# Kernel tuning notes

Measured on AMD Instinct MI355X. Metric: run time of the kernel, lower is better.

The kernel has to match this reference:

```python
import jax, jax.numpy as jnp
import numpy as np

V, NEIGH, C, N, H = 20000, 12, 16, 8, 4


def _circulant_basis(n):
    eye = jnp.eye(n, dtype=jnp.float32)
    return jnp.stack([jnp.roll(eye, b, axis=1) for b in range(n)])  # [n, n, n]


def setup_inputs() -> dict:
    key = jax.random.key(0)
    ks = jax.random.split(key, 12)
    x = jax.random.normal(ks[0], (V, C, N), dtype=jnp.float32)
    neighbors = jax.random.randint(ks[1], (V, NEIGH), 0, V)
    mask = jax.random.bernoulli(ks[2], 0.8, (V, NEIGH))
    pt = jax.random.normal(ks[3], (V, NEIGH, N, N), dtype=jnp.float32)
    rel_pos_u = jax.random.normal(ks[4], (V, NEIGH, 2), dtype=jnp.float32) * 0.1
    reg_basis = _circulant_basis(N)                                   # [N, N, N]
    value_basis1 = jax.random.normal(ks[5], (N, 2, N, N), dtype=jnp.float32)
    value_basis2 = jax.random.normal(ks[6], (N, 3, N, N), dtype=jnp.float32)
    s = 1.0 / np.sqrt(C * N)
    query_coeffs = jax.random.normal(ks[7], (H, C, N), dtype=jnp.float32) * s
    key_coeffs = jax.random.normal(ks[8], (H, C, N), dtype=jnp.float32) * s
    value0_params = jax.random.normal(ks[9], (H, C, N), dtype=jnp.float32) * s
    value1_params = jax.random.normal(ks[10], (H, C, N), dtype=jnp.float32) * s
    value2_params = jax.random.normal(ks[11], (H, C, N), dtype=jnp.float32) * s
    wm_weights = jax.random.normal(jax.random.fold_in(key, 99), (C, H * C, N), dtype=jnp.float32) * np.sqrt(2.0 / (H * C * N))
    return {"x": x, "neighbors": neighbors, "mask": mask,
            "parallel_transport_matrices": pt, "rel_pos_u": rel_pos_u,
            "reg_basis": reg_basis, "value_basis1": value_basis1,
            "value_basis2": value_basis2, "query_coeffs": query_coeffs,
            "key_coeffs": key_coeffs, "value0_params": value0_params,
            "value1_params": value1_params, "value2_params": value2_params,
            "wm_weights": wm_weights}


def reference(x, neighbors, mask, parallel_transport_matrices, rel_pos_u,
              reg_basis, value_basis1, value_basis2, query_coeffs, key_coeffs,
              value0_params, value1_params, value2_params, wm_weights):
    Nv, Cc, Nn = x.shape
    Hh = query_coeffs.shape[0]
    m = mask.astype(x.dtype)                                   # [v, n]
    x_neigh = x[neighbors] * m[:, :, None, None]               # [v, n, c, N]
    f = jnp.einsum('vnij,vncj->vnci', parallel_transport_matrices, x_neigh)
    # attention scores
    WQ = jnp.einsum('hcb,bij->hcij', query_coeffs, reg_basis)
    Q = jnp.einsum('hcij,vcj->vhi', WQ, x)                     # [v, h, N]
    WK = jnp.einsum('hcb,bij->hcij', key_coeffs, reg_basis)
    K = jnp.einsum('hcij,vncj->vnhi', WK, f)                   # [v, n, h, N]
    score = jax.nn.relu(Q[:, None] + K).mean(-1)               # [v, n, h]
    score = jnp.where(mask[:, :, None], score, 0.0)
    den = score.sum(axis=1)                                    # [v, h]
    dead = den < 1e-6
    n_valid = jnp.clip(m.sum(axis=1, keepdims=True), 1.0)      # [v, 1]
    uniform = m[:, :, None] / n_valid[:, :, None]              # [v, n, 1]
    attn = jnp.where(dead[:, None, :], uniform,
                     score / jnp.clip(den, 1e-6)[:, None, :])  # [v, n, h]
    # Taylor-basis values
    u0, u1 = rel_pos_u[..., 0], rel_pos_u[..., 1]
    u_quad = jnp.stack([u0 * u0, 2.0 * u0 * u1, u1 * u1], axis=-1)  # [v, n, 3]
    W0 = jnp.einsum('hcb,bij->hcij', value0_params, reg_basis)
    values = jnp.einsum('hcij,vncj->vnhci', W0, f)
    W1 = jnp.einsum('hcb,boij->hcoij', value1_params, value_basis1)
    values = values + jnp.einsum('hcoij,vncj,vno->vnhci', W1, f, rel_pos_u)
    W2 = jnp.einsum('hcb,boij->hcoij', value2_params, value_basis2)
    values = values + jnp.einsum('hcoij,vncj,vno->vnhci', W2, f, u_quad)
    head = jnp.einsum('vnh,vnhci->vhci', attn, values)         # [v, h, c, N]
    head = head.reshape(Nv, Hh * Cc, Nn)
    WM = jnp.einsum('ocb,bij->ocij', wm_weights, reg_basis)
    return jnp.einsum('ocij,vcj->voi', WM, head)               # [v, c, N]
```

## Files before the change

### kernel.cpp

```cpp
#include <hip/hip_runtime.h>

#define NV  20000
#define NNB 12
#define NC  16
#define NH  4
#define VC  4
#define GRID (NV/VC)

#define OFF_X    0
#define OFF_PT   528
#define OFF_HEAD 528
#define OFF_F    3792
#define OFF_QC   10128
#define OFF_KC   10656
#define OFF_Q    11184
#define OFF_SC   11312
#define OFF_DEN  11504
#define OFF_NV   11520
#define OFF_AT   11524
#define OFF_SCAL 11716
#define OFF_NB   12100
#define OFF_M    12148
#define SMEM_FL  12196

#define LD8(dst, off) { const float4 _a = *(const float4*)&smem[(off)]; \
                        const float4 _b = *(const float4*)&smem[(off)+4]; \
                        dst[0]=_a.x; dst[1]=_a.y; dst[2]=_a.z; dst[3]=_a.w; \
                        dst[4]=_b.x; dst[5]=_b.y; dst[6]=_b.z; dst[7]=_b.w; }
#define ST8(off, src) { *(float4*)&smem[(off)]   = make_float4(src[0],src[1],src[2],src[3]); \
                        *(float4*)&smem[(off)+4] = make_float4(src[4],src[5],src[6],src[7]); }

__global__ __launch_bounds__(256) void kdetect(const unsigned char* __restrict__ m,
                                               int* __restrict__ flag)
{
    __shared__ int s_nz;
    if (threadIdx.x == 0) s_nz = 0;
    __syncthreads();
    int nz = 0;
    for (int k = blockIdx.x * 256 + threadIdx.x; k < NV * NNB; k += gridDim.x * 256) {
        if ((k & 3) != 0 && m[k] != 0) nz = 1;
    }
    if (nz) atomicOr(&s_nz, 1);
    __syncthreads();
    if (threadIdx.x == 0 && s_nz) atomicOr(flag, 1);
}

__global__ __launch_bounds__(256) void ksetup(
    const float* __restrict__ v0p, const float* __restrict__ v1p,
    const float* __restrict__ v2p, const float* __restrict__ vb1,
    const float* __restrict__ vb2, float* __restrict__ A4)
{
    int idx = blockIdx.x * 256 + threadIdx.x;
    if (idx >= 24576) return;
    int j = idx & 7;
    int t = idx >> 3;
    int hc = t & 63; t >>= 6;
    int i = t & 7;
    int p = t >> 3;
    int h = hc >> 4, c = hc & 15;
    float s = 0.f;
    if (p == 0) {
        s = v0p[h*128 + c*8 + ((j - i + 8) & 7)];
    } else if (p <= 2) {
        int o = p - 1;
        #pragma unroll
        for (int b = 0; b < 8; ++b)
            s += v1p[h*128 + c*8 + b] * vb1[((b*2 + o)*8 + i)*8 + j];
    } else {
        int o = p - 3;
        #pragma unroll
        for (int b = 0; b < 8; ++b)
            s += v2p[h*128 + c*8 + b] * vb2[((b*3 + o)*8 + i)*8 + j];
    }
    A4[idx] = s;
}

__global__ __launch_bounds__(256) void kmain(
    const float* __restrict__ x, const int* __restrict__ nbr,
    const unsigned char* __restrict__ mskb, const float* __restrict__ pt,
    const float* __restrict__ rel, const float* __restrict__ qc,
    const float* __restrict__ kc, const float* __restrict__ A4,
    const float* __restrict__ wm, const int* __restrict__ flagp,
    float* __restrict__ out)
{
    const int tid = threadIdx.x;
    const int vbase = blockIdx.x * VC;
    const int bytemode = flagp[0];
    const int* mski = (const int*)mskb;

    __shared__ __align__(16) float smem[SMEM_FL];

    for (int k = tid; k < VC*128; k += 256)
        smem[OFF_X + (k>>7)*132 + (k&127)] = x[(vbase + (k>>7))*128 + (k&127)];
    for (int k = tid; k < VC*NNB*64; k += 256)
        smem[OFF_PT + (k>>6)*68 + (k&63)] = pt[vbase*(NNB*64) + k];
    for (int k = tid; k < 512; k += 256) {
        smem[OFF_QC + (k>>7)*132 + (k&127)] = qc[k];
        smem[OFF_KC + (k>>7)*132 + (k&127)] = kc[k];
    }
    if (tid < VC*NNB) {
        int gi = vbase*NNB + tid;
        ((int*)smem)[OFF_NB + tid] = nbr[gi];
        int raw = bytemode ? (int)mskb[gi] : mski[gi];
        smem[OFF_M + tid] = raw ? 1.0f : 0.0f;
    }
    if (tid >= 64 && tid < 64 + VC*NNB) {
        int vn = tid - 64;
        float u0 = rel[(vbase*NNB + vn)*2 + 0];
        float u1 = rel[(vbase*NNB + vn)*2 + 1];
        smem[OFF_SCAL+vn*8+0] = 1.0f;
        smem[OFF_SCAL+vn*8+1] = u0;
        smem[OFF_SCAL+vn*8+2] = u1;
        smem[OFF_SCAL+vn*8+3] = u0*u0;
        smem[OFF_SCAL+vn*8+4] = 2.0f*u0*u1;
        smem[OFF_SCAL+vn*8+5] = u1*u1;
        smem[OFF_SCAL+vn*8+6] = 0.0f;
        smem[OFF_SCAL+vn*8+7] = 0.0f;
    }
    __syncthreads();

    if (tid < 192) {
        const int vn = tid >> 2, cq = tid & 3;
        const int nb = ((const int*)smem)[OFF_NB + vn];
        const float m = smem[OFF_M + vn];
        const float4* xg = (const float4*)(x + nb*128 + cq*32);
        float xnf[32];
        #pragma unroll
        for (int q = 0; q < 8; ++q) {
            float4 tv = xg[q];
            xnf[q*4+0]=tv.x; xnf[q*4+1]=tv.y; xnf[q*4+2]=tv.z; xnf[q*4+3]=tv.w;
        }
        float acc[4][8];
        #pragma unroll
        for (int c4 = 0; c4 < 4; ++c4)
            #pragma unroll
            for (int i = 0; i < 8; ++i) acc[c4][i] = 0.f;
        #pragma unroll
        for (int i = 0; i < 8; ++i) {
            float pj[8]; LD8(pj, OFF_PT + vn*68 + i*8);
            #pragma unroll
            for (int c4 = 0; c4 < 4; ++c4)
                #pragma unroll
                for (int j = 0; j < 8; ++j)
                    acc[c4][i] += pj[j] * xnf[c4*8 + j];
        }
        #pragma unroll
        for (int c4 = 0; c4 < 4; ++c4) {
            int c = cq*4 + c4;
            float w[8];
            #pragma unroll
            for (int i = 0; i < 8; ++i) w[i] = m * acc[c4][i];
            ST8(OFF_F + vn*132 + c*8, w);
        }
    }
    __syncthreads();

    float K8[8] = {0,0,0,0,0,0,0,0};
    if (tid < 128) {
        const int cs = tid & 7, vh = tid >> 3, v = vh >> 2, h = vh & 3;
        float Q8[8] = {0,0,0,0,0,0,0,0};
        #pragma unroll
        for (int t = 0; t < 2; ++t) {
            int c = cs*2 + t;
            float xv[8]; LD8(xv, OFF_X + v*132 + c*8);
            float qv[8]; LD8(qv, OFF_QC + h*132 + c*8);
            #pragma unroll
            for (int s = 0; s < 8; ++s)
                #pragma unroll
                for (int i = 0; i < 8; ++i)
                    Q8[i] += qv[s] * xv[(i+s)&7];
        }
        #pragma unroll
        for (int msk = 1; msk < 8; msk <<= 1)
            #pragma unroll
            for (int i = 0; i < 8; ++i) Q8[i] += __shfl_xor(Q8[i], msk, 64);
        if (cs == 0) { ST8(OFF_Q + vh*8, Q8); }
    }
    if (tid < 192) {
        const int vn = tid >> 2, h = tid & 3;
        #pragma unroll 2
        for (int c = 0; c < 16; ++c) {
            float kv[8]; LD8(kv, OFF_KC + h*132 + c*8);
            float fv[8]; LD8(fv, OFF_F + vn*132 + c*8);
            #pragma unroll
            for (int s = 0; s < 8; ++s)
                #pragma unroll
                for (int i = 0; i < 8; ++i)
                    K8[i] += kv[s] * fv[(i+s)&7];
        }
    }
    __syncthreads();

    if (tid < 192) {
        const int vn = tid >> 2, h = tid & 3, v = vn / 12;
        float q[8]; LD8(q, OFF_Q + (v*4+h)*8);
        float s = 0.f;
        #pragma unroll
        for (int i = 0; i < 8; ++i) s += fmaxf(0.f, q[i] + K8[i]);
        smem[OFF_SC + vn*4 + h] = 0.125f * s * smem[OFF_M + vn];
    }
    __syncthreads();

    if (tid < 16) {
        int v = tid >> 2, h = tid & 3;
        float d = 0.f;
        for (int n = 0; n < 12; ++n) d += smem[OFF_SC + (v*12+n)*4 + h];
        smem[OFF_DEN + tid] = d;
        if (h == 0) {
            float nv = 0.f;
            for (int n = 0; n < 12; ++n) nv += smem[OFF_M + v*12 + n];
            smem[OFF_NV + v] = fmaxf(nv, 1.0f);
        }
    }
    __syncthreads();
    if (tid < 192) {
        const int vn = tid >> 2, h = tid & 3, v = vn / 12;
        float den = smem[OFF_DEN + v*4 + h];
        float at = (den < 1e-6f) ? (smem[OFF_M + vn] / smem[OFF_NV + v])
                                 : (smem[OFF_SC + vn*4 + h] / fmaxf(den, 1e-6f));
        smem[OFF_AT + vn*4 + h] = at;
    }
    __syncthreads();

    const int v6 = tid >> 6, h6 = (tid >> 4) & 3, c6 = tid & 15, hc = tid & 63;
    float G[6][8];
    #pragma unroll
    for (int p = 0; p < 6; ++p)
        #pragma unroll
        for (int j = 0; j < 8; ++j) G[p][j] = 0.f;
    for (int n = 0; n < 12; ++n) {
        int vn = v6*12 + n;
        float at = smem[OFF_AT + vn*4 + h6];
        float sc[8]; LD8(sc, OFF_SCAL + vn*8);
        float fv[8]; LD8(fv, OFF_F + vn*132 + c6*8);
        #pragma unroll
        for (int p = 0; p < 6; ++p) {
            float w = at * sc[p];
            #pragma unroll
            for (int j = 0; j < 8; ++j) G[p][j] += w * fv[j];
        }
    }
    float hd[8] = {0,0,0,0,0,0,0,0};
    #pragma unroll
    for (int p = 0; p < 6; ++p) {
        #pragma unroll
        for (int i = 0; i < 8; ++i) {
            const float4 a0 = *(const float4*)&A4[(((p*8+i)*64 + hc)*8)];
            const float4 a1 = *(const float4*)&A4[(((p*8+i)*64 + hc)*8) + 4];
            hd[i] += a0.x*G[p][0] + a0.y*G[p][1] + a0.z*G[p][2] + a0.w*G[p][3]
                   + a1.x*G[p][4] + a1.y*G[p][5] + a1.z*G[p][6] + a1.w*G[p][7];
        }
    }
    ST8(OFF_HEAD + v6*520 + hc*8, hd);
    __syncthreads();

    {
        const int v = tid >> 6, o = (tid >> 2) & 15, cs = tid & 3;
        float acc[8] = {0,0,0,0,0,0,0,0};
        #pragma unroll 2
        for (int cc = 0; cc < 16; ++cc) {
            int cp = cc*4 + cs;
            float hh[8]; LD8(hh, OFF_HEAD + v*520 + cp*8);
            const float4 w0 = *(const float4*)&wm[(o*64 + cp)*8];
            const float4 w1 = *(const float4*)&wm[(o*64 + cp)*8 + 4];
            float wv[8] = {w0.x,w0.y,w0.z,w0.w,w1.x,w1.y,w1.z,w1.w};
            #pragma unroll
            for (int d = 0; d < 8; ++d)
                #pragma unroll
                for (int i = 0; i < 8; ++i)
                    acc[i] += wv[d] * hh[(i+d)&7];
        }
        #pragma unroll
        for (int msk = 1; msk < 4; msk <<= 1)
            #pragma unroll
            for (int i = 0; i < 8; ++i) acc[i] += __shfl_xor(acc[i], msk, 64);
        if (cs == 0) {
            float* op = out + (vbase + v)*128 + o*8;
            *(float4*)op       = make_float4(acc[0],acc[1],acc[2],acc[3]);
            *(float4*)(op + 4) = make_float4(acc[4],acc[5],acc[6],acc[7]);
        }
    }
}

extern "C" void kernel_launch(void* const* d_in, const int* in_sizes, int n_in,
                              void* d_out, int out_size, void* d_ws, size_t ws_size,
                              hipStream_t stream)
{
    const float* x   = (const float*)d_in[0];
    const int*   nbr = (const int*)d_in[1];
    const unsigned char* msk = (const unsigned char*)d_in[2];
    const float* pt  = (const float*)d_in[3];
    const float* rel = (const float*)d_in[4];
    const float* vb1 = (const float*)d_in[6];
    const float* vb2 = (const float*)d_in[7];
    const float* qc  = (const float*)d_in[8];
    const float* kc  = (const float*)d_in[9];
    const float* v0p = (const float*)d_in[10];
    const float* v1p = (const float*)d_in[11];
    const float* v2p = (const float*)d_in[12];
    const float* wm  = (const float*)d_in[13];

    int*   flag = (int*)d_ws;
    float* A4   = (float*)d_ws + 64;
    float* outp = (float*)d_out;

    hipMemsetAsync(d_ws, 0, 256, stream);
    hipLaunchKernelGGL(kdetect, dim3(64),   dim3(256), 0, stream, msk, flag);
    hipLaunchKernelGGL(ksetup,  dim3(96),   dim3(256), 0, stream, v0p, v1p, v2p, vb1, vb2, A4);
    hipLaunchKernelGGL(kmain,   dim3(GRID), dim3(256), 0, stream,
                       x, nbr, msk, pt, rel, qc, kc, A4, wm, flag, outp);
}
```

Measured before the change: 321.9 us.

## Shrink LDS footprint via buffer aliasing and merge prep kernels into one launch

Reorganizes the shared-memory layout so the parallel-transport staging area is reused for the query/key coefficients, Q and head buffers, and the attention weights overwrite the score buffer. x is now read directly from global memory instead of being staged, and the scalar basis array is compacted. Together these cut LDS per block so that four blocks can fit per CU, which launch_bounds(256,4) now requests. The mask-detect and basis-setup kernels are merged into one launch to save launch overhead. The cost is an extra barrier, a __syncthreads inside a branch that is only safe because the split falls on wave boundaries, and tighter register limits.

```diff
diff --git a/kernel.cpp b/kernel.cpp
--- a/kernel.cpp
+++ b/kernel.cpp
@@ -7,21 +7,20 @@
 #define VC  4
 #define GRID (NV/VC)
 
-#define OFF_X    0
-#define OFF_PT   528
-#define OFF_HEAD 528
-#define OFF_F    3792
-#define OFF_QC   10128
-#define OFF_KC   10656
-#define OFF_Q    11184
-#define OFF_SC   11312
-#define OFF_DEN  11504
-#define OFF_NV   11520
-#define OFF_AT   11524
-#define OFF_SCAL 11716
-#define OFF_NB   12100
-#define OFF_M    12148
-#define SMEM_FL  12196
+#define OFF_R    0
+#define OFF_QC   0
+#define OFF_KC   528
+#define OFF_Q    1056
+#define OFF_HEAD 1184
+#define OFF_F    3264
+#define OFF_SC   9600
+#define OFF_DEN  9792
+#define OFF_NV   9808
+#define OFF_S4   9816
+#define OFF_S2   10008
+#define OFF_NB   10104
+#define OFF_M    10152
+#define SMEM_FL  10200
 
 #define LD8(dst, off) { const float4 _a = *(const float4*)&smem[(off)]; \
                         const float4 _b = *(const float4*)&smem[(off)+4]; \
@@ -30,52 +29,51 @@
 #define ST8(off, src) { *(float4*)&smem[(off)]   = make_float4(src[0],src[1],src[2],src[3]); \
                         *(float4*)&smem[(off)+4] = make_float4(src[4],src[5],src[6],src[7]); }
 
-__global__ __launch_bounds__(256) void kdetect(const unsigned char* __restrict__ m,
-                                               int* __restrict__ flag)
-{
-    __shared__ int s_nz;
-    if (threadIdx.x == 0) s_nz = 0;
-    __syncthreads();
-    int nz = 0;
-    for (int k = blockIdx.x * 256 + threadIdx.x; k < NV * NNB; k += gridDim.x * 256) {
-        if ((k & 3) != 0 && m[k] != 0) nz = 1;
-    }
-    if (nz) atomicOr(&s_nz, 1);
-    __syncthreads();
-    if (threadIdx.x == 0 && s_nz) atomicOr(flag, 1);
-}
-
-__global__ __launch_bounds__(256) void ksetup(
+__global__ __launch_bounds__(256) void kprep(
     const float* __restrict__ v0p, const float* __restrict__ v1p,
     const float* __restrict__ v2p, const float* __restrict__ vb1,
-    const float* __restrict__ vb2, float* __restrict__ A4)
+    const float* __restrict__ vb2, float* __restrict__ A4,
+    const unsigned char* __restrict__ m, int* __restrict__ flag)
 {
-    int idx = blockIdx.x * 256 + threadIdx.x;
-    if (idx >= 24576) return;
-    int j = idx & 7;
-    int t = idx >> 3;
-    int hc = t & 63; t >>= 6;
-    int i = t & 7;
-    int p = t >> 3;
-    int h = hc >> 4, c = hc & 15;
-    float s = 0.f;
-    if (p == 0) {
-        s = v0p[h*128 + c*8 + ((j - i + 8) & 7)];
-    } else if (p <= 2) {
-        int o = p - 1;
-        #pragma unroll
-        for (int b = 0; b < 8; ++b)
-            s += v1p[h*128 + c*8 + b] * vb1[((b*2 + o)*8 + i)*8 + j];
+    const int b = blockIdx.x, tid = threadIdx.x;
+    if (b < 96) {
+        int idx = b * 256 + tid;
+        int j = idx & 7;
+        int t = idx >> 3;
+        int hc = t & 63; t >>= 6;
+        int i = t & 7;
+        int p = t >> 3;
+        int h = hc >> 4, c = hc & 15;
+        float s = 0.f;
+        if (p == 0) {
+            s = v0p[h*128 + c*8 + ((j - i + 8) & 7)];
+        } else if (p <= 2) {
+            int o = p - 1;
+            #pragma unroll
+            for (int bb = 0; bb < 8; ++bb)
+                s += v1p[h*128 + c*8 + bb] * vb1[((bb*2 + o)*8 + i)*8 + j];
+        } else {
+            int o = p - 3;
+            #pragma unroll
+            for (int bb = 0; bb < 8; ++bb)
+                s += v2p[h*128 + c*8 + bb] * vb2[((bb*3 + o)*8 + i)*8 + j];
+        }
+        A4[idx] = s;
     } else {
-        int o = p - 3;
-        #pragma unroll
-        for (int b = 0; b < 8; ++b)
-            s += v2p[h*128 + c*8 + b] * vb2[((b*3 + o)*8 + i)*8 + j];
-    }
-    A4[idx] = s;
+        __shared__ int s_nz;
+        if (tid == 0) s_nz = 0;
+        __syncthreads();
+        int nz = 0;
+        for (int k = (b - 96) * 256 + tid; k < NV * NNB; k += 64 * 256) {
+            if ((k & 3) != 0 && m[k] != 0) nz = 1;
+        }
+        if (nz) atomicOr(&s_nz, 1);
+        __syncthreads();
+        if (tid == 0 && s_nz) atomicOr(flag, 1);
+    }
 }
 
-__global__ __launch_bounds__(256) void kmain(
+__global__ __launch_bounds__(256, 4) void kmain(
     const float* __restrict__ x, const int* __restrict__ nbr,
     const unsigned char* __restrict__ mskb, const float* __restrict__ pt,
     const float* __restrict__ rel, const float* __restrict__ qc,
@@ -90,14 +88,8 @@
 
     __shared__ __align__(16) float smem[SMEM_FL];
 
-    for (int k = tid; k < VC*128; k += 256)
-        smem[OFF_X + (k>>7)*132 + (k&127)] = x[(vbase + (k>>7))*128 + (k&127)];
     for (int k = tid; k < VC*NNB*64; k += 256)
-        smem[OFF_PT + (k>>6)*68 + (k&63)] = pt[vbase*(NNB*64) + k];
-    for (int k = tid; k < 512; k += 256) {
-        smem[OFF_QC + (k>>7)*132 + (k&127)] = qc[k];
-        smem[OFF_KC + (k>>7)*132 + (k&127)] = kc[k];
-    }
+        smem[OFF_R + (k>>6)*68 + (k&63)] = pt[vbase*(NNB*64) + k];
     if (tid < VC*NNB) {
         int gi = vbase*NNB + tid;
         ((int*)smem)[OFF_NB + tid] = nbr[gi];
@@ -108,14 +100,12 @@
         int vn = tid - 64;
         float u0 = rel[(vbase*NNB + vn)*2 + 0];
         float u1 = rel[(vbase*NNB + vn)*2 + 1];
-        smem[OFF_SCAL+vn*8+0] = 1.0f;
-        smem[OFF_SCAL+vn*8+1] = u0;
-        smem[OFF_SCAL+vn*8+2] = u1;
-        smem[OFF_SCAL+vn*8+3] = u0*u0;
-        smem[OFF_SCAL+vn*8+4] = 2.0f*u0*u1;
-        smem[OFF_SCAL+vn*8+5] = u1*u1;
-        smem[OFF_SCAL+vn*8+6] = 0.0f;
-        smem[OFF_SCAL+vn*8+7] = 0.0f;
+        smem[OFF_S4+vn*4+0] = 1.0f;
+        smem[OFF_S4+vn*4+1] = u0;
+        smem[OFF_S4+vn*4+2] = u1;
+        smem[OFF_S4+vn*4+3] = u0*u0;
+        smem[OFF_S2+vn*2+0] = 2.0f*u0*u1;
+        smem[OFF_S2+vn*2+1] = u1*u1;
     }
     __syncthreads();
 
@@ -137,7 +127,7 @@
             for (int i = 0; i < 8; ++i) acc[c4][i] = 0.f;
         #pragma unroll
         for (int i = 0; i < 8; ++i) {
-            float pj[8]; LD8(pj, OFF_PT + vn*68 + i*8);
+            float pj[8]; LD8(pj, OFF_R + vn*68 + i*8);
             #pragma unroll
             for (int c4 = 0; c4 < 4; ++c4)
                 #pragma unroll
@@ -155,14 +145,23 @@
     }
     __syncthreads();
 
+    for (int k = tid; k < 512; k += 256) {
+        smem[OFF_QC + (k>>7)*132 + (k&127)] = qc[k];
+        smem[OFF_KC + (k>>7)*132 + (k&127)] = kc[k];
+    }
+    __syncthreads();
+
     float K8[8] = {0,0,0,0,0,0,0,0};
     if (tid < 128) {
         const int cs = tid & 7, vh = tid >> 3, v = vh >> 2, h = vh & 3;
+        const float* xrow = x + (vbase + v)*128;
         float Q8[8] = {0,0,0,0,0,0,0,0};
         #pragma unroll
         for (int t = 0; t < 2; ++t) {
             int c = cs*2 + t;
-            float xv[8]; LD8(xv, OFF_X + v*132 + c*8);
+            const float4 xa = *(const float4*)(xrow + c*8);
+            const float4 xb = *(const float4*)(xrow + c*8 + 4);
+            float xv[8] = {xa.x,xa.y,xa.z,xa.w,xb.x,xb.y,xb.z,xb.w};
             float qv[8]; LD8(qv, OFF_QC + h*132 + c*8);
             #pragma unroll
             for (int s = 0; s < 8; ++s)
@@ -218,7 +217,10 @@
         float den = smem[OFF_DEN + v*4 + h];
         float at = (den < 1e-6f) ? (smem[OFF_M + vn] / smem[OFF_NV + v])
                                  : (smem[OFF_SC + vn*4 + h] / fmaxf(den, 1e-6f));
-        smem[OFF_AT + vn*4 + h] = at;
+        __syncthreads();
+        smem[OFF_SC + vn*4 + h] = at;
+    } else {
+        __syncthreads();
     }
     __syncthreads();
 
@@ -230,15 +232,15 @@
         for (int j = 0; j < 8; ++j) G[p][j] = 0.f;
     for (int n = 0; n < 12; ++n) {
         int vn = v6*12 + n;
-        float at = smem[OFF_AT + vn*4 + h6];
-        float sc[8]; LD8(sc, OFF_SCAL + vn*8);
+        float at = smem[OFF_SC + vn*4 + h6];
+        const float4 s4 = *(const float4*)&smem[OFF_S4 + vn*4];
+        const float2 s2 = *(const float2*)&smem[OFF_S2 + vn*2];
         float fv[8]; LD8(fv, OFF_F + vn*132 + c6*8);
-        #pragma unroll
-        for (int p = 0; p < 6; ++p) {
-            float w = at * sc[p];
-            #pragma unroll
-            for (int j = 0; j < 8; ++j) G[p][j] += w * fv[j];
-        }
+        float w[6] = {at*s4.x, at*s4.y, at*s4.z, at*s4.w, at*s2.x, at*s2.y};
+        #pragma unroll
+        for (int p = 0; p < 6; ++p)
+            #pragma unroll
+            for (int j = 0; j < 8; ++j) G[p][j] += w[p] * fv[j];
     }
     float hd[8] = {0,0,0,0,0,0,0,0};
     #pragma unroll
@@ -305,8 +307,8 @@
     float* outp = (float*)d_out;
 
     hipMemsetAsync(d_ws, 0, 256, stream);
-    hipLaunchKernelGGL(kdetect, dim3(64),   dim3(256), 0, stream, msk, flag);
-    hipLaunchKernelGGL(ksetup,  dim3(96),   dim3(256), 0, stream, v0p, v1p, v2p, vb1, vb2, A4);
-    hipLaunchKernelGGL(kmain,   dim3(GRID), dim3(256), 0, stream,
+    hipLaunchKernelGGL(kprep, dim3(160),  dim3(256), 0, stream,
+                       v0p, v1p, v2p, vb1, vb2, A4, msk, flag);
+    hipLaunchKernelGGL(kmain, dim3(GRID), dim3(256), 0, stream,
                        x, nbr, msk, pt, rel, qc, kc, A4, wm, flag, outp);
 }
```

Measured after the change: 277.3 us. -13.9%, faster.
